# Performance work log

Hardware: AMD Instinct MI355X
Metric: run time of the kernel (lower is better)

The kernel has to match this reference:

```python
import jax, jax.numpy as jnp
import numpy as np

N = 100000        # nodes
E = 1600000       # edges
G = 1000          # graphs
DIM = 256         # dim_h
DEPTH = 4
VOCAB = 100
MAX_ND = 20
EPS = 1e-5


def setup_inputs() -> dict:
    key = jax.random.key(0)
    ks = jax.random.split(key, 24)
    inp = {
        "x_idx": jax.random.randint(ks[0], (N,), 0, VOCAB, dtype=jnp.int32),
        "node_depth": jax.random.randint(ks[1], (N,), 0, MAX_ND, dtype=jnp.int32),
        "edge_index": jax.random.randint(ks[2], (2, E), 0, N, dtype=jnp.int32),
        "batch": jnp.sort(jax.random.randint(ks[3], (N,), 0, G, dtype=jnp.int32)),
        # node encoder embeddings
        "emb_node": 0.02 * jax.random.normal(ks[4], (VOCAB, DIM), jnp.float32),
        "emb_depth": 0.02 * jax.random.normal(ks[5], (MAX_ND, DIM), jnp.float32),
        # per-depth GIN MLP: Linear(DIM,DIM) -> ReLU -> Linear(DIM,DIM)
        "gin_w1": 0.05 * jax.random.normal(ks[6], (DEPTH, DIM, DIM), jnp.float32),
        "gin_b1": jnp.zeros((DEPTH, DIM), jnp.float32),
        "gin_w2": 0.05 * jax.random.normal(ks[7], (DEPTH, DIM, DIM), jnp.float32),
        "gin_b2": jnp.zeros((DEPTH, DIM), jnp.float32),
        # GraphNorm params
        "gn_alpha": jnp.ones((DEPTH, DIM), jnp.float32),
        "gn_gamma": jnp.ones((DEPTH, DIM), jnp.float32),
        "gn_beta": jnp.zeros((DEPTH, DIM), jnp.float32),
        # attention gate MLP: Linear(DIM, 2*DIM) -> ReLU -> Linear(2*DIM, 1)
        "att_w1": 0.05 * jax.random.normal(ks[8], (DEPTH, DIM, 2 * DIM), jnp.float32),
        "att_b1": jnp.zeros((DEPTH, 2 * DIM), jnp.float32),
        "att_w2": 0.05 * jax.random.normal(ks[9], (DEPTH, 2 * DIM, 1), jnp.float32),
        "att_b2": jnp.zeros((DEPTH, 1), jnp.float32),
    }
    return inp


def _graph_norm(x, batch, alpha, gamma, beta):
    # per-graph GraphNorm (Cai et al.): shift by alpha*mean, scale by std
    cnt = jax.ops.segment_sum(jnp.ones((x.shape[0],), x.dtype), batch, num_segments=G)
    cnt = jnp.maximum(cnt, 1.0)[:, None]                     # [G,1]
    mean = jax.ops.segment_sum(x, batch, num_segments=G) / cnt
    out = x - alpha * mean[batch]
    var = jax.ops.segment_sum(out * out, batch, num_segments=G) / cnt
    inv = jax.lax.rsqrt(var + EPS)
    return gamma * out * inv[batch] + beta


def _att_pool(x, batch, w1, b1, w2, b2):
    gate = (jax.nn.relu(x @ w1 + b1) @ w2 + b2)[:, 0]        # [N]
    m = jax.ops.segment_max(gate, batch, num_segments=G)
    e = jnp.exp(gate - m[batch])
    denom = jax.ops.segment_sum(e, batch, num_segments=G)
    w = e / denom[batch]                                     # segment softmax
    return jax.ops.segment_sum(w[:, None] * x, batch, num_segments=G)  # [G,DIM]


def reference(x_idx, node_depth, edge_index, batch,
              emb_node, emb_depth,
              gin_w1, gin_b1, gin_w2, gin_b2,
              gn_alpha, gn_gamma, gn_beta,
              att_w1, att_b1, att_w2, att_b2):
    src, dst = edge_index[0], edge_index[1]
    x = emb_node[x_idx] + emb_depth[node_depth]              # node encoder [N,DIM]
    graph_embs = []
    for d in range(DEPTH):
        x_in = x
        # GINConv (eps=0): MLP(x + sum_{j->i} x_j)
        agg = jax.ops.segment_sum(x[src], dst, num_segments=N)
        h = x + agg
        x = jax.nn.relu(h @ gin_w1[d] + gin_b1[d]) @ gin_w2[d] + gin_b2[d]
        x = _graph_norm(x, batch, gn_alpha[d], gn_gamma[d], gn_beta[d])
        if d < DEPTH - 1:
            x = jax.nn.relu(x)
        x = x + x_in                                         # residual
        graph_embs.append(_att_pool(x, batch, att_w1[d], att_b1[d], att_w2[d], att_b2[d]))
    stacked = jnp.stack(graph_embs, axis=0)                  # [DEPTH,G,DIM]
    agg_emb = jnp.mean(stacked, axis=0)                      # MLAP-Mean aggregate
    return jnp.concatenate([stacked, agg_emb[None]], axis=0) # [DEPTH+1,G,DIM]
```

## Files before the change

kernel.cpp:

```cpp
#include <hip/hip_runtime.h>
#include <hip/hip_bf16.h>

#define NN 100000
#define EE 1600000
#define GG 1000
#define DIMH 256
#define NDEPTH 4
static constexpr float EPSV = 1e-5f;

typedef unsigned short ushort;
typedef __attribute__((ext_vector_type(8))) ushort ushort8v;
typedef __attribute__((ext_vector_type(8))) short short8v;
typedef __attribute__((ext_vector_type(4))) float f32x4;

__device__ __forceinline__ float bf2f(ushort u) {
    return __uint_as_float(((unsigned)u) << 16);
}
__device__ __forceinline__ ushort f2bf(float f) {
    unsigned u = __float_as_uint(f);
    unsigned r = u + 0x7FFFu + ((u >> 16) & 1u);
    return (ushort)(r >> 16);
}

#define GLOAD16(g, s) __builtin_amdgcn_global_load_lds((const __attribute__((address_space(1))) void*)(g), \
                      (__attribute__((address_space(3))) void*)(s), 16, 0, 0)

__global__ __launch_bounds__(256) void k_graph_bounds(const int* __restrict__ batch, int* __restrict__ gstart) {
    int g = blockIdx.x * 256 + threadIdx.x;
    if (g > GG) return;
    int lo = 0, hi = NN;
    while (lo < hi) { int mid = (lo + hi) >> 1; if (batch[mid] < g) lo = mid + 1; else hi = mid; }
    gstart[g] = lo;
}

__global__ __launch_bounds__(256) void k_hist(const int* __restrict__ dst, int* __restrict__ deg) {
    int e = blockIdx.x * 256 + threadIdx.x;
    if (e < EE) atomicAdd(&deg[dst[e]], 1);
}

__global__ __launch_bounds__(256) void k_scan_a(const int* __restrict__ deg, int* __restrict__ rs, int* __restrict__ part) {
    __shared__ int s[256];
    int t = threadIdx.x;
    int i = blockIdx.x * 256 + t;
    int v = (i < NN) ? deg[i] : 0;
    s[t] = v; __syncthreads();
    for (int off = 1; off < 256; off <<= 1) {
        int u = (t >= off) ? s[t - off] : 0;
        __syncthreads();
        s[t] += u;
        __syncthreads();
    }
    if (i < NN) rs[i] = s[t] - v;
    if (t == 255) part[blockIdx.x] = s[255];
}

__global__ __launch_bounds__(512) void k_scan_b(int* __restrict__ part, int nb, int* __restrict__ rs) {
    __shared__ int s[512];
    int t = threadIdx.x;
    int v = (t < nb) ? part[t] : 0;
    s[t] = v; __syncthreads();
    for (int off = 1; off < 512; off <<= 1) {
        int u = (t >= off) ? s[t - off] : 0;
        __syncthreads();
        s[t] += u;
        __syncthreads();
    }
    if (t < nb) part[t] = s[t] - v;
    if (t == 0) rs[NN] = EE;
}

__global__ __launch_bounds__(256) void k_scan_c(int* __restrict__ rs, const int* __restrict__ part) {
    int i = blockIdx.x * 256 + threadIdx.x;
    if (i < NN) rs[i] += part[blockIdx.x];
}

__global__ __launch_bounds__(256) void k_copy_int(const int* __restrict__ a, int* __restrict__ b, int n) {
    int i = blockIdx.x * 256 + threadIdx.x;
    if (i < n) b[i] = a[i];
}

__global__ __launch_bounds__(256) void k_scatter(const int* __restrict__ src, const int* __restrict__ dst,
                                                 int* __restrict__ cursor, int* __restrict__ col) {
    int e = blockIdx.x * 256 + threadIdx.x;
    if (e >= EE) return;
    int d = dst[e];
    int pos = atomicAdd(&cursor[d], 1);
    col[pos] = src[e];
}

__global__ __launch_bounds__(256) void k_wtrans(const float* __restrict__ in, ushort* __restrict__ out_hi,
                                                ushort* __restrict__ out_lo, int K, int N) {
    int d = blockIdx.z;
    in  += (size_t)d * K * N;
    out_hi += (size_t)d * K * N;
    out_lo += (size_t)d * K * N;
    int n0 = blockIdx.x * 32, k0 = blockIdx.y * 32;
    int t = threadIdx.x;
    int tx = t & 31, ty = t >> 5;
    __shared__ float tile[32][33];
#pragma unroll
    for (int j = 0; j < 4; j++) tile[ty + 8 * j][tx] = in[(size_t)(k0 + ty + 8 * j) * N + n0 + tx];
    __syncthreads();
#pragma unroll
    for (int j = 0; j < 4; j++) {
        float f = tile[tx][ty + 8 * j];
        ushort hi = f2bf(f);
        float lo = f - bf2f(hi);
        size_t o = (size_t)(n0 + ty + 8 * j) * K + k0 + tx;
        out_hi[o] = hi;
        out_lo[o] = f2bf(lo);
    }
}

__global__ __launch_bounds__(256) void k_encoder(const int* __restrict__ xidx, const int* __restrict__ ndep,
                                                 const float* __restrict__ en, const float* __restrict__ ed,
                                                 ushort* __restrict__ x) {
    int gi = blockIdx.x * 256 + threadIdx.x;
    int node = gi >> 6, q = gi & 63;
    if (node >= NN) return;
    float4 va = ((const float4*)en)[(size_t)xidx[node] * 64 + q];
    float4 vb = ((const float4*)ed)[(size_t)ndep[node] * 64 + q];
    ushort4 o;
    o.x = f2bf(va.x + vb.x); o.y = f2bf(va.y + vb.y);
    o.z = f2bf(va.z + vb.z); o.w = f2bf(va.w + vb.w);
    ((ushort4*)x)[gi] = o;
}

__global__ __launch_bounds__(256) void k_aggregate(const ushort* __restrict__ x, const int* __restrict__ rs,
                                                   const int* __restrict__ col, ushort* __restrict__ hb) {
    int node = blockIdx.x * 4 + (threadIdx.x >> 6);
    int lane = threadIdx.x & 63;
    if (node >= NN) return;
    const ushort4* x4 = (const ushort4*)x;
    ushort4 sv = x4[(size_t)node * 64 + lane];
    float a0 = bf2f(sv.x), a1 = bf2f(sv.y), a2 = bf2f(sv.z), a3 = bf2f(sv.w);
    float b0 = 0.f, b1 = 0.f, b2 = 0.f, b3 = 0.f;
    float c0 = 0.f, c1 = 0.f, c2 = 0.f, c3 = 0.f;
    float d0 = 0.f, d1 = 0.f, d2 = 0.f, d3 = 0.f;
    int s = rs[node], e = rs[node + 1];
    int j = s;
    for (; j + 8 <= e; j += 8) {
        int i0 = col[j], i1 = col[j + 1], i2 = col[j + 2], i3 = col[j + 3];
        int i4 = col[j + 4], i5 = col[j + 5], i6 = col[j + 6], i7 = col[j + 7];
        ushort4 v0 = x4[(size_t)i0 * 64 + lane];
        ushort4 v1 = x4[(size_t)i1 * 64 + lane];
        ushort4 v2 = x4[(size_t)i2 * 64 + lane];
        ushort4 v3 = x4[(size_t)i3 * 64 + lane];
        ushort4 v4 = x4[(size_t)i4 * 64 + lane];
        ushort4 v5 = x4[(size_t)i5 * 64 + lane];
        ushort4 v6 = x4[(size_t)i6 * 64 + lane];
        ushort4 v7 = x4[(size_t)i7 * 64 + lane];
        a0 += bf2f(v0.x); a1 += bf2f(v0.y); a2 += bf2f(v0.z); a3 += bf2f(v0.w);
        b0 += bf2f(v1.x); b1 += bf2f(v1.y); b2 += bf2f(v1.z); b3 += bf2f(v1.w);
        c0 += bf2f(v2.x); c1 += bf2f(v2.y); c2 += bf2f(v2.z); c3 += bf2f(v2.w);
        d0 += bf2f(v3.x); d1 += bf2f(v3.y); d2 += bf2f(v3.z); d3 += bf2f(v3.w);
        a0 += bf2f(v4.x); a1 += bf2f(v4.y); a2 += bf2f(v4.z); a3 += bf2f(v4.w);
        b0 += bf2f(v5.x); b1 += bf2f(v5.y); b2 += bf2f(v5.z); b3 += bf2f(v5.w);
        c0 += bf2f(v6.x); c1 += bf2f(v6.y); c2 += bf2f(v6.z); c3 += bf2f(v6.w);
        d0 += bf2f(v7.x); d1 += bf2f(v7.y); d2 += bf2f(v7.z); d3 += bf2f(v7.w);
    }
    for (; j + 4 <= e; j += 4) {
        int i0 = col[j], i1 = col[j + 1], i2 = col[j + 2], i3 = col[j + 3];
        ushort4 v0 = x4[(size_t)i0 * 64 + lane];
        ushort4 v1 = x4[(size_t)i1 * 64 + lane];
        ushort4 v2 = x4[(size_t)i2 * 64 + lane];
        ushort4 v3 = x4[(size_t)i3 * 64 + lane];
        a0 += bf2f(v0.x); a1 += bf2f(v0.y); a2 += bf2f(v0.z); a3 += bf2f(v0.w);
        b0 += bf2f(v1.x); b1 += bf2f(v1.y); b2 += bf2f(v1.z); b3 += bf2f(v1.w);
        c0 += bf2f(v2.x); c1 += bf2f(v2.y); c2 += bf2f(v2.z); c3 += bf2f(v2.w);
        d0 += bf2f(v3.x); d1 += bf2f(v3.y); d2 += bf2f(v3.z); d3 += bf2f(v3.w);
    }
    for (; j < e; j++) {
        int c = col[j];
        ushort4 v = x4[(size_t)c * 64 + lane];
        a0 += bf2f(v.x); a1 += bf2f(v.y); a2 += bf2f(v.z); a3 += bf2f(v.w);
    }
    a0 += b0 + c0 + d0; a1 += b1 + c1 + d1; a2 += b2 + c2 + d2; a3 += b3 + c3 + d3;
    ushort4 o; o.x = f2bf(a0); o.y = f2bf(a1); o.z = f2bf(a2); o.w = f2bf(a3);
    ((ushort4*)hb)[(size_t)node * 64 + lane] = o;
}

template<int MODE>
__global__ __launch_bounds__(256, 2) void k_mfma_gemm(const ushort* __restrict__ A,
                                                      const ushort* __restrict__ Bhi,
                                                      const ushort* __restrict__ Blo,
                                                      const float* __restrict__ bias,
                                                      const float* __restrict__ w2,
                                                      ushort* __restrict__ C,
                                                      float* __restrict__ partial,
                                                      int M) {
    __shared__ __align__(16) ushort lds[2 * 16384];
    int t = threadIdx.x;
    int wv = t >> 6, l = t & 63;
    int wr = wv >> 1, wc = wv & 1;
    int row0 = blockIdx.x * 256;
    int col0 = blockIdx.y * 128;

    f32x4 acc[8][4];
#pragma unroll
    for (int m = 0; m < 8; m++)
#pragma unroll
        for (int n = 0; n < 4; n++) acc[m][n] = (f32x4){0.f, 0.f, 0.f, 0.f};

    int srow = l >> 2;
    int sck  = ((l & 3) ^ ((l >> 3) & 3)) * 8;

    auto stage = [&](int k0, ushort* buf) {
#pragma unroll
        for (int i = 0; i < 4; i++) {
            int stripe = wv * 4 + i;
            int rl = stripe * 16 + srow;
            const ushort* ga = A + (size_t)min(row0 + rl, M - 1) * 256 + k0 + sck;
            GLOAD16(ga, buf + stripe * 512 + l * 8);
        }
#pragma unroll
        for (int i = 0; i < 2; i++) {
            int stripe = wv * 2 + i;
            int rl = stripe * 16 + srow;
            const ushort* gh = Bhi + (size_t)(col0 + rl) * 256 + k0 + sck;
            GLOAD16(gh, buf + 8192 + stripe * 512 + l * 8);
            const ushort* gl = Blo + (size_t)(col0 + rl) * 256 + k0 + sck;
            GLOAD16(gl, buf + 12288 + stripe * 512 + l * 8);
        }
    };

    int lr = l & 15, kc = l >> 4;

    ushort* cur = lds;
    ushort* nxt = lds + 16384;
    stage(0, cur);
    __syncthreads();

    for (int it = 0; it < 8; it++) {
        if (it < 7) stage((it + 1) * 32, nxt);

        short8v af[8], bhf[4], blf[4];
#pragma unroll
        for (int m = 0; m < 8; m++) {
            int r = wr * 128 + m * 16 + lr;
            af[m] = *(const short8v*)(cur + r * 32 + ((kc ^ ((r >> 1) & 3)) * 8));
        }
#pragma unroll
        for (int n = 0; n < 4; n++) {
            int rb = wc * 64 + n * 16 + lr;
            int so = (kc ^ ((rb >> 1) & 3)) * 8;
            bhf[n] = *(const short8v*)(cur + 8192 + rb * 32 + so);
            blf[n] = *(const short8v*)(cur + 12288 + rb * 32 + so);
        }
#pragma unroll
        for (int m = 0; m < 8; m++)
#pragma unroll
            for (int n = 0; n < 4; n++) {
                acc[m][n] = __builtin_amdgcn_mfma_f32_16x16x32_bf16(af[m], bhf[n], acc[m][n], 0, 0, 0);
                acc[m][n] = __builtin_amdgcn_mfma_f32_16x16x32_bf16(af[m], blf[n], acc[m][n], 0, 0, 0);
            }
        __syncthreads();
        ushort* tmp = cur; cur = nxt; nxt = tmp;
    }

    if (MODE == 2) {
        float b1v[4], w2v[4];
#pragma unroll
        for (int n = 0; n < 4; n++) {
            int colc = col0 + wc * 64 + n * 16 + lr;
            b1v[n] = bias[colc];
            w2v[n] = w2[colc];
        }
#pragma unroll
        for (int m = 0; m < 8; m++) {
#pragma unroll
            for (int j = 0; j < 4; j++) {
                float p = 0.f;
#pragma unroll
                for (int n = 0; n < 4; n++) {
                    float v = fmaxf(acc[m][n][j] + b1v[n], 0.f);
                    p = fmaf(v, w2v[n], p);
                }
#pragma unroll
                for (int off = 1; off < 16; off <<= 1) p += __shfl_xor(p, off, 64);
                if (lr == 0) {
                    int row = row0 + wr * 128 + m * 16 + (kc << 2) + j;
                    if (row < M) partial[(size_t)row * 8 + blockIdx.y * 2 + wc] = p;
                }
            }
        }
    } else {
        float bv[4];
#pragma unroll
        for (int n = 0; n < 4; n++) bv[n] = bias[col0 + wc * 64 + n * 16 + lr];
#pragma unroll
        for (int m = 0; m < 8; m++) {
#pragma unroll
            for (int j = 0; j < 4; j++) {
                int row = row0 + wr * 128 + m * 16 + (kc << 2) + j;
                if (row < M) {
#pragma unroll
                    for (int n = 0; n < 4; n++) {
                        float v = acc[m][n][j] + bv[n];
                        if (MODE == 1) v = fmaxf(v, 0.f);
                        C[(size_t)row * 256 + col0 + wc * 64 + n * 16 + lr] = f2bf(v);
                    }
                }
            }
        }
    }
}

__global__ __launch_bounds__(256) void k_gatefin(const float* __restrict__ partial, const float* __restrict__ b2,
                                                 float* __restrict__ gate) {
    int i = blockIdx.x * 256 + threadIdx.x;
    if (i >= NN) return;
    const float4* p = (const float4*)(partial + (size_t)i * 8);
    float4 u = p[0], v = p[1];
    gate[i] = u.x + u.y + u.z + u.w + v.x + v.y + v.z + v.w + b2[0];
}

__global__ __launch_bounds__(256) void k_statsnorm(const ushort* __restrict__ y, const int* __restrict__ gstart,
                                                   const float* __restrict__ alpha, const float* __restrict__ gamma,
                                                   const float* __restrict__ beta, ushort* __restrict__ x, int relu) {
    int g = blockIdx.x, t = threadIdx.x;
    int s = gstart[g], e = gstart[g + 1];
    if (s >= e) return;
    float s1 = 0.f, s2 = 0.f;
    for (int i = s; i < e; i++) {
        float v = bf2f(y[(size_t)i * DIMH + t]);
        s1 += v; s2 = fmaf(v, v, s2);
    }
    float cnt = (float)((e - s) > 1 ? (e - s) : 1);
    float m = s1 / cnt;
    float a = alpha[t];
    float am = a * m;
    float var = s2 / cnt - 2.f * am * m + am * am;
    float iv = rsqrtf(var + EPSV);
    float ga = gamma[t], be = beta[t];
    for (int i = s; i < e; i++) {
        float v  = bf2f(y[(size_t)i * DIMH + t]);
        float xo = bf2f(x[(size_t)i * DIMH + t]);
        float o = (v - am) * iv * ga + be;
        if (relu) o = fmaxf(o, 0.f);
        x[(size_t)i * DIMH + t] = f2bf(xo + o);
    }
}

__global__ __launch_bounds__(256) void k_pool(const ushort* __restrict__ x, const float* __restrict__ gate,
                                              const int* __restrict__ gstart, float* __restrict__ outg) {
    __shared__ float red[256];
    __shared__ float wbuf[256];
    int g = blockIdx.x, t = threadIdx.x;
    int s = gstart[g], e = gstart[g + 1];
    if (s >= e) { outg[(size_t)g * DIMH + t] = 0.f; return; }
    float m = -3.4e38f;
    for (int i = s + t; i < e; i += 256) m = fmaxf(m, gate[i]);
    red[t] = m; __syncthreads();
    for (int o = 128; o > 0; o >>= 1) { if (t < o) red[t] = fmaxf(red[t], red[t + o]); __syncthreads(); }
    m = red[0]; __syncthreads();
    float se = 0.f;
    for (int i = s + t; i < e; i += 256) se += expf(gate[i] - m);
    red[t] = se; __syncthreads();
    for (int o = 128; o > 0; o >>= 1) { if (t < o) red[t] += red[t + o]; __syncthreads(); }
    float inv_se = 1.f / red[0];
    float o_acc = 0.f;
    for (int base = s; base < e; base += 256) {
        __syncthreads();
        int i = base + t;
        wbuf[t] = (i < e) ? expf(gate[i] - m) * inv_se : 0.f;
        __syncthreads();
        int cnt = min(256, e - base);
        for (int j = 0; j < cnt; j++) o_acc += wbuf[j] * bf2f(x[(size_t)(base + j) * DIMH + t]);
    }
    outg[(size_t)g * DIMH + t] = o_acc;
}

__global__ __launch_bounds__(256) void k_final(float* __restrict__ out) {
    const int GD = GG * DIMH;
    int i = blockIdx.x * 256 + threadIdx.x;
    if (i >= GD) return;
    float s = out[i] + out[GD + i] + out[2 * GD + i] + out[3 * GD + i];
    out[4 * GD + i] = 0.25f * s;
}

__global__ __launch_bounds__(256) void k_zero_out(float* __restrict__ out, int n) {
    int i = blockIdx.x * 256 + threadIdx.x;
    if (i < n) out[i] = 0.f;
}

extern "C" void kernel_launch(void* const* d_in, const int* in_sizes, int n_in,
                              void* d_out, int out_size, void* d_ws, size_t ws_size,
                              hipStream_t stream) {
    const int*   x_idx     = (const int*)d_in[0];
    const int*   node_dep  = (const int*)d_in[1];
    const int*   eidx      = (const int*)d_in[2];
    const int*   batch     = (const int*)d_in[3];
    const float* emb_node  = (const float*)d_in[4];
    const float* emb_depth = (const float*)d_in[5];
    const float* gin_w1    = (const float*)d_in[6];
    const float* gin_b1    = (const float*)d_in[7];
    const float* gin_w2    = (const float*)d_in[8];
    const float* gin_b2    = (const float*)d_in[9];
    const float* gn_alpha  = (const float*)d_in[10];
    const float* gn_gamma  = (const float*)d_in[11];
    const float* gn_beta   = (const float*)d_in[12];
    const float* att_w1    = (const float*)d_in[13];
    const float* att_b1    = (const float*)d_in[14];
    const float* att_w2    = (const float*)d_in[15];
    const float* att_b2    = (const float*)d_in[16];
    float* out = (float*)d_out;
    (void)in_sizes; (void)n_in;

    const size_t SZ_NODE_BF16 = (size_t)NN * DIMH * 2;
    const size_t SZ_W256 = (size_t)NDEPTH * 256 * 256 * 2;
    const size_t SZ_W512 = (size_t)NDEPTH * 256 * 512 * 2;
    size_t required = 3 * ((SZ_NODE_BF16 + 255) & ~(size_t)255)
                    + 4 * SZ_W256 + 2 * SZ_W512
                    + ((size_t)EE * 4 + 256) + ((size_t)(NN + 1) * 4 + 256) * 2
                    + 4096 + 8192 + ((size_t)NN * 4 + 256) + 65536;
    if (ws_size < required) {
        k_zero_out<<<(out_size + 255) / 256, 256, 0, stream>>>(out, out_size);
        return;
    }

    char* w = (char*)d_ws;
    size_t off = 0;
    auto alloc = [&](size_t bytes) -> char* {
        char* p = w + off;
        off += (bytes + 255) & ~(size_t)255;
        return p;
    };
    ushort* x  = (ushort*)alloc(SZ_NODE_BF16);
    ushort* hb = (ushort*)alloc(SZ_NODE_BF16);
    ushort* y1 = (ushort*)alloc(SZ_NODE_BF16);
    float* partial = (float*)y1;
    ushort* wt_g1h = (ushort*)alloc(SZ_W256);
    ushort* wt_g1l = (ushort*)alloc(SZ_W256);
    ushort* wt_g2h = (ushort*)alloc(SZ_W256);
    ushort* wt_g2l = (ushort*)alloc(SZ_W256);
    ushort* wt_a1h = (ushort*)alloc(SZ_W512);
    ushort* wt_a1l = (ushort*)alloc(SZ_W512);
    int* deg    = (int*)alloc((size_t)NN * 4);
    int* rs     = (int*)alloc((size_t)(NN + 1) * 4);
    int* part   = (int*)alloc(512 * 4);
    int* gstart = (int*)alloc((GG + 1) * 4);
    int* col    = (int*)alloc((size_t)EE * 4);
    float* gate = (float*)alloc((size_t)NN * 4);

    const int* src  = eidx;
    const int* dstp = eidx + EE;

    hipMemsetAsync(deg, 0, (size_t)NN * 4, stream);
    k_graph_bounds<<<(GG + 1 + 255) / 256, 256, 0, stream>>>(batch, gstart);
    k_hist<<<(EE + 255) / 256, 256, 0, stream>>>(dstp, deg);
    int nb = (NN + 255) / 256;
    k_scan_a<<<nb, 256, 0, stream>>>(deg, rs, part);
    k_scan_b<<<1, 512, 0, stream>>>(part, nb, rs);
    k_scan_c<<<nb, 256, 0, stream>>>(rs, part);
    k_copy_int<<<nb, 256, 0, stream>>>(rs, deg, NN);
    k_scatter<<<(EE + 255) / 256, 256, 0, stream>>>(src, dstp, deg, col);
    k_encoder<<<(NN * 64 + 255) / 256, 256, 0, stream>>>(x_idx, node_dep, emb_node, emb_depth, x);

    k_wtrans<<<dim3(8, 8, NDEPTH), 256, 0, stream>>>(gin_w1, wt_g1h, wt_g1l, 256, 256);
    k_wtrans<<<dim3(8, 8, NDEPTH), 256, 0, stream>>>(gin_w2, wt_g2h, wt_g2l, 256, 256);
    k_wtrans<<<dim3(16, 8, NDEPTH), 256, 0, stream>>>(att_w1, wt_a1h, wt_a1l, 256, 512);

    const int GD = GG * DIMH;
    const int MB = (NN + 255) / 256;
    for (int d = 0; d < NDEPTH; d++) {
        k_aggregate<<<(NN + 3) / 4, 256, 0, stream>>>(x, rs, col, hb);
        k_mfma_gemm<1><<<dim3(MB, 2), 256, 0, stream>>>(hb, wt_g1h + (size_t)d * 65536, wt_g1l + (size_t)d * 65536,
                                                        gin_b1 + d * 256, nullptr, y1, nullptr, NN);
        k_mfma_gemm<0><<<dim3(MB, 2), 256, 0, stream>>>(y1, wt_g2h + (size_t)d * 65536, wt_g2l + (size_t)d * 65536,
                                                        gin_b2 + d * 256, nullptr, hb, nullptr, NN);
        k_statsnorm<<<GG, 256, 0, stream>>>(hb, gstart, gn_alpha + d * 256, gn_gamma + d * 256,
                                            gn_beta + d * 256, x, (d < NDEPTH - 1) ? 1 : 0);
        k_mfma_gemm<2><<<dim3(MB, 4), 256, 0, stream>>>(x, wt_a1h + (size_t)d * 131072, wt_a1l + (size_t)d * 131072,
                                                        att_b1 + d * 512, att_w2 + d * 512, nullptr, partial, NN);
        k_gatefin<<<(NN + 255) / 256, 256, 0, stream>>>(partial, att_b2 + d, gate);
        k_pool<<<GG, 256, 0, stream>>>(x, gate, gstart, out + (size_t)d * GD);
    }
    k_final<<<(GD + 255) / 256, 256, 0, stream>>>(out);
}
```

Baseline: 1.670 ms.

## Bucket edges before CSR scatter, use K=64 GEMM tiles, cache GraphNorm rows in LDS

CSR construction now first sorts edges into 256-node buckets by destination, then scatters them into the final CSR from the bucketed buffer. This gives the final atomic scatter better locality and removes the separate histogram and copy kernels. The MFMA GEMM drops its double-buffered K=32 pipeline for single-buffered K=64 tiles with a new XOR swizzle, so there are fewer barriers but load and compute no longer overlap. GraphNorm caches up to 144 rows per graph in shared memory so the second pass does not reread them from global memory. The larger LDS footprint may lower occupancy.

```diff
diff --git a/kernel.cpp b/kernel.cpp
--- a/kernel.cpp
+++ b/kernel.cpp
@@ -6,10 +6,11 @@
 #define GG 1000
 #define DIMH 256
 #define NDEPTH 4
+#define NBUCK 391
+#define LDSROWS 144
 static constexpr float EPSV = 1e-5f;
 
 typedef unsigned short ushort;
-typedef __attribute__((ext_vector_type(8))) ushort ushort8v;
 typedef __attribute__((ext_vector_type(8))) short short8v;
 typedef __attribute__((ext_vector_type(4))) float f32x4;
 
@@ -33,9 +34,36 @@
     gstart[g] = lo;
 }
 
-__global__ __launch_bounds__(256) void k_hist(const int* __restrict__ dst, int* __restrict__ deg) {
+__global__ __launch_bounds__(256) void k_bhist(const int* __restrict__ dst, int* __restrict__ bcnt) {
     int e = blockIdx.x * 256 + threadIdx.x;
-    if (e < EE) atomicAdd(&deg[dst[e]], 1);
+    if (e < EE) atomicAdd(&bcnt[dst[e] >> 8], 1);
+}
+
+__global__ __launch_bounds__(512) void k_bscan(const int* __restrict__ bcnt, int* __restrict__ bstart,
+                                               int* __restrict__ bcursor) {
+    __shared__ int s[512];
+    int t = threadIdx.x;
+    int v = (t < NBUCK) ? bcnt[t] : 0;
+    s[t] = v; __syncthreads();
+    for (int off = 1; off < 512; off <<= 1) {
+        int u = (t >= off) ? s[t - off] : 0;
+        __syncthreads();
+        s[t] += u;
+        __syncthreads();
+    }
+    if (t < NBUCK) { int ex = s[t] - v; bstart[t] = ex; bcursor[t] = ex; }
+    if (t == 0) bstart[NBUCK] = EE;
+}
+
+__global__ __launch_bounds__(256) void k_bscatter(const int* __restrict__ src, const int* __restrict__ dst,
+                                                  int* __restrict__ bcursor, int2* __restrict__ ebuf,
+                                                  int* __restrict__ deg) {
+    int e = blockIdx.x * 256 + threadIdx.x;
+    if (e >= EE) return;
+    int d = dst[e];
+    int pos = atomicAdd(&bcursor[d >> 8], 1);
+    ebuf[pos] = make_int2(src[e], d);
+    atomicAdd(&deg[d], 1);
 }
 
 __global__ __launch_bounds__(256) void k_scan_a(const int* __restrict__ deg, int* __restrict__ rs, int* __restrict__ part) {
@@ -69,23 +97,23 @@
     if (t == 0) rs[NN] = EE;
 }
 
-__global__ __launch_bounds__(256) void k_scan_c(int* __restrict__ rs, const int* __restrict__ part) {
+__global__ __launch_bounds__(256) void k_scan_c(int* __restrict__ rs, const int* __restrict__ part,
+                                                int* __restrict__ cursor) {
     int i = blockIdx.x * 256 + threadIdx.x;
-    if (i < NN) rs[i] += part[blockIdx.x];
-}
-
-__global__ __launch_bounds__(256) void k_copy_int(const int* __restrict__ a, int* __restrict__ b, int n) {
-    int i = blockIdx.x * 256 + threadIdx.x;
-    if (i < n) b[i] = a[i];
-}
-
-__global__ __launch_bounds__(256) void k_scatter(const int* __restrict__ src, const int* __restrict__ dst,
-                                                 int* __restrict__ cursor, int* __restrict__ col) {
+    if (i < NN) {
+        int v = rs[i] + part[blockIdx.x];
+        rs[i] = v;
+        cursor[i] = v;
+    }
+}
+
+__global__ __launch_bounds__(256) void k_scatter2(const int2* __restrict__ ebuf, int* __restrict__ cursor,
+                                                  int* __restrict__ col) {
     int e = blockIdx.x * 256 + threadIdx.x;
     if (e >= EE) return;
-    int d = dst[e];
-    int pos = atomicAdd(&cursor[d], 1);
-    col[pos] = src[e];
+    int2 p = ebuf[e];
+    int pos = atomicAdd(&cursor[p.y], 1);
+    col[pos] = p.x;
 }
 
 __global__ __launch_bounds__(256) void k_wtrans(const float* __restrict__ in, ushort* __restrict__ out_hi,
@@ -181,15 +209,17 @@
 }
 
 template<int MODE>
-__global__ __launch_bounds__(256, 2) void k_mfma_gemm(const ushort* __restrict__ A,
-                                                      const ushort* __restrict__ Bhi,
-                                                      const ushort* __restrict__ Blo,
-                                                      const float* __restrict__ bias,
-                                                      const float* __restrict__ w2,
-                                                      ushort* __restrict__ C,
-                                                      float* __restrict__ partial,
-                                                      int M) {
-    __shared__ __align__(16) ushort lds[2 * 16384];
+__global__ __launch_bounds__(256, 2) void k_gemm64(const ushort* __restrict__ A,
+                                                   const ushort* __restrict__ Bhi,
+                                                   const ushort* __restrict__ Blo,
+                                                   const float* __restrict__ bias,
+                                                   const float* __restrict__ w2,
+                                                   ushort* __restrict__ C,
+                                                   float* __restrict__ partial,
+                                                   int M) {
+    __shared__ __align__(16) ushort As[256 * 64];
+    __shared__ __align__(16) ushort Bh[128 * 64];
+    __shared__ __align__(16) ushort Bl[128 * 64];
     int t = threadIdx.x;
     int wv = t >> 6, l = t & 63;
     int wr = wv >> 1, wc = wv & 1;
@@ -202,62 +232,57 @@
 #pragma unroll
         for (int n = 0; n < 4; n++) acc[m][n] = (f32x4){0.f, 0.f, 0.f, 0.f};
 
-    int srow = l >> 2;
-    int sck  = ((l & 3) ^ ((l >> 3) & 3)) * 8;
-
-    auto stage = [&](int k0, ushort* buf) {
+    int srow_in = l >> 3;
+    int slot    = l & 7;
+
+    for (int k0 = 0; k0 < 256; k0 += 64) {
+#pragma unroll
+        for (int i = 0; i < 8; i++) {
+            int stripe = wv * 8 + i;
+            int rl = stripe * 8 + srow_in;
+            int gc = slot ^ (rl & 7);
+            const ushort* ga = A + (size_t)min(row0 + rl, M - 1) * 256 + k0 + gc * 8;
+            GLOAD16(ga, As + stripe * 512 + l * 8);
+        }
 #pragma unroll
         for (int i = 0; i < 4; i++) {
             int stripe = wv * 4 + i;
-            int rl = stripe * 16 + srow;
-            const ushort* ga = A + (size_t)min(row0 + rl, M - 1) * 256 + k0 + sck;
-            GLOAD16(ga, buf + stripe * 512 + l * 8);
+            int rl = stripe * 8 + srow_in;
+            int gc = slot ^ (rl & 7);
+            const ushort* gh = Bhi + (size_t)(col0 + rl) * 256 + k0 + gc * 8;
+            GLOAD16(gh, Bh + stripe * 512 + l * 8);
+            const ushort* gl = Blo + (size_t)(col0 + rl) * 256 + k0 + gc * 8;
+            GLOAD16(gl, Bl + stripe * 512 + l * 8);
         }
-#pragma unroll
-        for (int i = 0; i < 2; i++) {
-            int stripe = wv * 2 + i;
-            int rl = stripe * 16 + srow;
-            const ushort* gh = Bhi + (size_t)(col0 + rl) * 256 + k0 + sck;
-            GLOAD16(gh, buf + 8192 + stripe * 512 + l * 8);
-            const ushort* gl = Blo + (size_t)(col0 + rl) * 256 + k0 + sck;
-            GLOAD16(gl, buf + 12288 + stripe * 512 + l * 8);
+        __syncthreads();
+#pragma unroll
+        for (int s = 0; s < 2; s++) {
+            short8v af[8], bhf[4], blf[4];
+#pragma unroll
+            for (int m = 0; m < 8; m++) {
+                int r = wr * 128 + m * 16 + (l & 15);
+                int ch = (s * 4 + (l >> 4)) ^ (r & 7);
+                af[m] = *(const short8v*)(As + r * 64 + ch * 8);
+            }
+#pragma unroll
+            for (int n = 0; n < 4; n++) {
+                int rb = wc * 64 + n * 16 + (l & 15);
+                int ch = (s * 4 + (l >> 4)) ^ (rb & 7);
+                bhf[n] = *(const short8v*)(Bh + rb * 64 + ch * 8);
+                blf[n] = *(const short8v*)(Bl + rb * 64 + ch * 8);
+            }
+#pragma unroll
+            for (int m = 0; m < 8; m++)
+#pragma unroll
+                for (int n = 0; n < 4; n++) {
+                    acc[m][n] = __builtin_amdgcn_mfma_f32_16x16x32_bf16(af[m], bhf[n], acc[m][n], 0, 0, 0);
+                    acc[m][n] = __builtin_amdgcn_mfma_f32_16x16x32_bf16(af[m], blf[n], acc[m][n], 0, 0, 0);
+                }
         }
-    };
+        __syncthreads();
+    }
 
     int lr = l & 15, kc = l >> 4;
-
-    ushort* cur = lds;
-    ushort* nxt = lds + 16384;
-    stage(0, cur);
-    __syncthreads();
-
-    for (int it = 0; it < 8; it++) {
-        if (it < 7) stage((it + 1) * 32, nxt);
-
-        short8v af[8], bhf[4], blf[4];
-#pragma unroll
-        for (int m = 0; m < 8; m++) {
-            int r = wr * 128 + m * 16 + lr;
-            af[m] = *(const short8v*)(cur + r * 32 + ((kc ^ ((r >> 1) & 3)) * 8));
-        }
-#pragma unroll
-        for (int n = 0; n < 4; n++) {
-            int rb = wc * 64 + n * 16 + lr;
-            int so = (kc ^ ((rb >> 1) & 3)) * 8;
-            bhf[n] = *(const short8v*)(cur + 8192 + rb * 32 + so);
-            blf[n] = *(const short8v*)(cur + 12288 + rb * 32 + so);
-        }
-#pragma unroll
-        for (int m = 0; m < 8; m++)
-#pragma unroll
-            for (int n = 0; n < 4; n++) {
-                acc[m][n] = __builtin_amdgcn_mfma_f32_16x16x32_bf16(af[m], bhf[n], acc[m][n], 0, 0, 0);
-                acc[m][n] = __builtin_amdgcn_mfma_f32_16x16x32_bf16(af[m], blf[n], acc[m][n], 0, 0, 0);
-            }
-        __syncthreads();
-        ushort* tmp = cur; cur = nxt; nxt = tmp;
-    }
-
     if (MODE == 2) {
         float b1v[4], w2v[4];
 #pragma unroll
@@ -318,27 +343,31 @@
 __global__ __launch_bounds__(256) void k_statsnorm(const ushort* __restrict__ y, const int* __restrict__ gstart,
                                                    const float* __restrict__ alpha, const float* __restrict__ gamma,
                                                    const float* __restrict__ beta, ushort* __restrict__ x, int relu) {
+    __shared__ ushort yc[LDSROWS * DIMH];
     int g = blockIdx.x, t = threadIdx.x;
     int s = gstart[g], e = gstart[g + 1];
-    if (s >= e) return;
+    int n = e - s;
+    if (n <= 0) return;
     float s1 = 0.f, s2 = 0.f;
-    for (int i = s; i < e; i++) {
-        float v = bf2f(y[(size_t)i * DIMH + t]);
+    for (int r = 0; r < n; r++) {
+        ushort raw = y[(size_t)(s + r) * DIMH + t];
+        if (r < LDSROWS) yc[r * DIMH + t] = raw;
+        float v = bf2f(raw);
         s1 += v; s2 = fmaf(v, v, s2);
     }
-    float cnt = (float)((e - s) > 1 ? (e - s) : 1);
+    float cnt = (float)(n > 1 ? n : 1);
     float m = s1 / cnt;
     float a = alpha[t];
     float am = a * m;
     float var = s2 / cnt - 2.f * am * m + am * am;
     float iv = rsqrtf(var + EPSV);
     float ga = gamma[t], be = beta[t];
-    for (int i = s; i < e; i++) {
-        float v  = bf2f(y[(size_t)i * DIMH + t]);
-        float xo = bf2f(x[(size_t)i * DIMH + t]);
+    for (int r = 0; r < n; r++) {
+        float v = (r < LDSROWS) ? bf2f(yc[r * DIMH + t]) : bf2f(y[(size_t)(s + r) * DIMH + t]);
+        float xo = bf2f(x[(size_t)(s + r) * DIMH + t]);
         float o = (v - am) * iv * ga + be;
         if (relu) o = fmaxf(o, 0.f);
-        x[(size_t)i * DIMH + t] = f2bf(xo + o);
+        x[(size_t)(s + r) * DIMH + t] = f2bf(xo + o);
     }
 }
 
@@ -413,7 +442,7 @@
     size_t required = 3 * ((SZ_NODE_BF16 + 255) & ~(size_t)255)
                     + 4 * SZ_W256 + 2 * SZ_W512
                     + ((size_t)EE * 4 + 256) + ((size_t)(NN + 1) * 4 + 256) * 2
-                    + 4096 + 8192 + ((size_t)NN * 4 + 256) + 65536;
+                    + 4096 + 16384 + ((size_t)NN * 4 + 256) + 65536;
     if (ws_size < required) {
         k_zero_out<<<(out_size + 255) / 256, 256, 0, stream>>>(out, out_size);
         return;
@@ -430,6 +459,7 @@
     ushort* hb = (ushort*)alloc(SZ_NODE_BF16);
     ushort* y1 = (ushort*)alloc(SZ_NODE_BF16);
     float* partial = (float*)y1;
+    int2* ebuf = (int2*)y1;
     ushort* wt_g1h = (ushort*)alloc(SZ_W256);
     ushort* wt_g1l = (ushort*)alloc(SZ_W256);
     ushort* wt_g2h = (ushort*)alloc(SZ_W256);
@@ -440,6 +470,9 @@
     int* rs     = (int*)alloc((size_t)(NN + 1) * 4);
     int* part   = (int*)alloc(512 * 4);
     int* gstart = (int*)alloc((GG + 1) * 4);
+    int* bcnt   = (int*)alloc((NBUCK + 1) * 4);
+    int* bstart = (int*)alloc((NBUCK + 1) * 4);
+    int* bcursor= (int*)alloc((NBUCK + 1) * 4);
     int* col    = (int*)alloc((size_t)EE * 4);
     float* gate = (float*)alloc((size_t)NN * 4);
 
@@ -447,14 +480,16 @@
     const int* dstp = eidx + EE;
 
     hipMemsetAsync(deg, 0, (size_t)NN * 4, stream);
+    hipMemsetAsync(bcnt, 0, (NBUCK + 1) * 4, stream);
     k_graph_bounds<<<(GG + 1 + 255) / 256, 256, 0, stream>>>(batch, gstart);
-    k_hist<<<(EE + 255) / 256, 256, 0, stream>>>(dstp, deg);
+    k_bhist<<<(EE + 255) / 256, 256, 0, stream>>>(dstp, bcnt);
+    k_bscan<<<1, 512, 0, stream>>>(bcnt, bstart, bcursor);
+    k_bscatter<<<(EE + 255) / 256, 256, 0, stream>>>(src, dstp, bcursor, ebuf, deg);
     int nb = (NN + 255) / 256;
     k_scan_a<<<nb, 256, 0, stream>>>(deg, rs, part);
     k_scan_b<<<1, 512, 0, stream>>>(part, nb, rs);
-    k_scan_c<<<nb, 256, 0, stream>>>(rs, part);
-    k_copy_int<<<nb, 256, 0, stream>>>(rs, deg, NN);
-    k_scatter<<<(EE + 255) / 256, 256, 0, stream>>>(src, dstp, deg, col);
+    k_scan_c<<<nb, 256, 0, stream>>>(rs, part, deg);
+    k_scatter2<<<(EE + 255) / 256, 256, 0, stream>>>(ebuf, deg, col);
     k_encoder<<<(NN * 64 + 255) / 256, 256, 0, stream>>>(x_idx, node_dep, emb_node, emb_depth, x);
 
     k_wtrans<<<dim3(8, 8, NDEPTH), 256, 0, stream>>>(gin_w1, wt_g1h, wt_g1l, 256, 256);
@@ -465,14 +500,14 @@
     const int MB = (NN + 255) / 256;
     for (int d = 0; d < NDEPTH; d++) {
         k_aggregate<<<(NN + 3) / 4, 256, 0, stream>>>(x, rs, col, hb);
-        k_mfma_gemm<1><<<dim3(MB, 2), 256, 0, stream>>>(hb, wt_g1h + (size_t)d * 65536, wt_g1l + (size_t)d * 65536,
-                                                        gin_b1 + d * 256, nullptr, y1, nullptr, NN);
-        k_mfma_gemm<0><<<dim3(MB, 2), 256, 0, stream>>>(y1, wt_g2h + (size_t)d * 65536, wt_g2l + (size_t)d * 65536,
-                                                        gin_b2 + d * 256, nullptr, hb, nullptr, NN);
+        k_gemm64<1><<<dim3(MB, 2), 256, 0, stream>>>(hb, wt_g1h + (size_t)d * 65536, wt_g1l + (size_t)d * 65536,
+                                                     gin_b1 + d * 256, nullptr, y1, nullptr, NN);
+        k_gemm64<0><<<dim3(MB, 2), 256, 0, stream>>>(y1, wt_g2h + (size_t)d * 65536, wt_g2l + (size_t)d * 65536,
+                                                     gin_b2 + d * 256, nullptr, hb, nullptr, NN);
         k_statsnorm<<<GG, 256, 0, stream>>>(hb, gstart, gn_alpha + d * 256, gn_gamma + d * 256,
                                             gn_beta + d * 256, x, (d < NDEPTH - 1) ? 1 : 0);
-        k_mfma_gemm<2><<<dim3(MB, 4), 256, 0, stream>>>(x, wt_a1h + (size_t)d * 131072, wt_a1l + (size_t)d * 131072,
-                                                        att_b1 + d * 512, att_w2 + d * 512, nullptr, partial, NN);
+        k_gemm64<2><<<dim3(MB, 4), 256, 0, stream>>>(x, wt_a1h + (size_t)d * 131072, wt_a1l + (size_t)d * 131072,
+                                                     att_b1 + d * 512, att_w2 + d * 512, nullptr, partial, NN);
         k_gatefin<<<(NN + 255) / 256, 256, 0, stream>>>(partial, att_b2 + d, gate);
         k_pool<<<GG, 256, 0, stream>>>(x, gate, gstart, out + (size_t)d * GD);
     }
```

New measurement: 3.027 ms. 81.2% more time.
